# Kernel optimization log

Hardware: AMD Instinct MI355X
Metric: run time of the kernel (lower is better)

The kernel has to match this reference:

```python
import jax, jax.numpy as jnp
import numpy as np

N_NODES = 50000
N_EDGES = 800000
D_IN = 128
D_OUT = 128


def setup_inputs() -> dict:
    key = jax.random.key(0)
    k1, k2, k3 = jax.random.split(key, 3)
    x = jax.random.normal(k1, (N_NODES, D_IN), dtype=jnp.float32)
    edge_index = jax.random.randint(k2, (2, N_EDGES), 0, N_NODES, dtype=jnp.int64)
    # glorot init for weight, zeros for bias
    limit = float(np.sqrt(6.0 / (D_IN + D_OUT)))
    W = jax.random.uniform(k3, (D_IN, D_OUT), dtype=jnp.float32, minval=-limit, maxval=limit)
    b = jnp.zeros((D_OUT,), dtype=jnp.float32)
    return {"x": x, "edge_index": edge_index, "W": W, "b": b}


def reference(x, edge_index, W, b):
    # GCNConv forward: dense transform, then sym-normalized propagation with self-loops.
    N = x.shape[0]
    h = x @ W  # [N, D_OUT]

    src = edge_index[0]
    dst = edge_index[1]
    # add self loops (fill weight = 1.0 since improved=False)
    loop = jnp.arange(N, dtype=src.dtype)
    src = jnp.concatenate([src, loop])
    dst = jnp.concatenate([dst, loop])
    ew = jnp.ones(src.shape[0], dtype=h.dtype)

    # sym normalization: D^{-1/2} A D^{-1/2}
    deg = jax.ops.segment_sum(ew, dst, num_segments=N)  # [N]
    deg_inv_sqrt = jnp.where(deg > 0, jax.lax.rsqrt(jnp.maximum(deg, 1e-12)), 0.0)
    norm = deg_inv_sqrt[src] * ew * deg_inv_sqrt[dst]  # [E+N]

    # message = norm * x_j ; aggregate = scatter-add to dst
    msg = norm[:, None] * h[src]  # [E+N, D_OUT]
    out = jax.ops.segment_sum(msg, dst, num_segments=N)  # [N, D_OUT]
    return out + b
```

## Files before the change

### kernel.cpp

```cpp
#include <hip/hip_runtime.h>
#include <math.h>

#define N_NODES 50000
#define N_EDGES 800000
#define D 128
#define NBKT 392
#define CHUNK 4096
#define NCHUNK ((N_EDGES + CHUNK - 1) / CHUNK)
#define CAPB 4096
#define GEMM_BLOCKS ((N_NODES + 63) / 64)

typedef short bf16x8 __attribute__((ext_vector_type(8)));
typedef float f32x4 __attribute__((ext_vector_type(4)));

static __device__ __forceinline__ unsigned short f2bf_rn(float f) {
    unsigned u = __float_as_uint(f);
    unsigned r = (u + 0x7FFF + ((u >> 16) & 1)) >> 16;
    return (unsigned short)r;
}
static __device__ __forceinline__ float bf2f(unsigned short h) {
    return __uint_as_float(((unsigned)h) << 16);
}


__global__ __launch_bounds__(256) void setup(const float* __restrict__ W,
                                             unsigned short* __restrict__ wH,
                                             int* __restrict__ gcur,
                                             int* __restrict__ row_start) {
    if (blockIdx.x < 8) {
        int tid = blockIdx.x * 256 + threadIdx.x;
        int kstep = tid >> 9;
        int ct = (tid >> 6) & 7;
        int lane = tid & 63;
        int kbase = kstep * 32 + ((lane >> 4) << 3);
        int c = ct * 16 + (lane & 15);
        #pragma unroll
        for (int e = 0; e < 8; ++e) {
            wH[tid * 8 + e] = f2bf_rn(W[(kbase + e) * 128 + c]);
        }
    } else {
        for (int j = threadIdx.x; j < NBKT; j += 256) gcur[j] = j * CAPB;
        if (threadIdx.x == 0) row_start[N_NODES] = N_EDGES;
    }
}


__global__ __launch_bounds__(256) void part_gemm(const int* __restrict__ ei,
                                                 int* __restrict__ gcur,
                                                 unsigned int* __restrict__ part,
                                                 const float* __restrict__ x,
                                                 const unsigned short* __restrict__ wH,
                                                 unsigned short* __restrict__ h) {
    __shared__ unsigned int ebuf[CHUNK];
    __shared__ unsigned int obuf[CHUNK];
    __shared__ int hist[NBKT];
    __shared__ int spos[NBKT];
    __shared__ int goff[NBKT];
    __shared__ int sm[256];
    int t = threadIdx.x;

    if (blockIdx.x < NCHUNK) {
        int base = blockIdx.x * CHUNK;
        int n = N_EDGES - base; if (n > CHUNK) n = CHUNK;

        for (int j = t; j < NBKT; j += 256) hist[j] = 0;
        __syncthreads();
        for (int i = t; i < n; i += 256) {
            unsigned s = (unsigned)ei[base + i];
            unsigned d = (unsigned)ei[N_EDGES + base + i];
            ebuf[i] = s | (d << 16);
            atomicAdd(&hist[d >> 7], 1);
        }
        __syncthreads();
        int i0 = 2 * t, i1 = i0 + 1;
        int a = (i0 < NBKT) ? hist[i0] : 0;
        int b = (i1 < NBKT) ? hist[i1] : 0;
        int ps = a + b;
        sm[t] = ps; __syncthreads();
        for (int o = 1; o < 256; o <<= 1) {
            int ad = (t >= o) ? sm[t - o] : 0;
            __syncthreads();
            sm[t] += ad;
            __syncthreads();
        }
        int ex = sm[t] - ps;
        if (i0 < NBKT) spos[i0] = ex;
        if (i1 < NBKT) spos[i1] = ex + a;
        __syncthreads();
        for (int j = t; j < NBKT; j += 256) {
            int gp = atomicAdd(&gcur[j], hist[j]);
            goff[j] = gp - spos[j];
        }
        __syncthreads();
        for (int j = t; j < NBKT; j += 256) hist[j] = 0;
        __syncthreads();
        for (int i = t; i < n; i += 256) {
            unsigned e = ebuf[i];
            int bk = e >> 23;
            int p = spos[bk] + atomicAdd(&hist[bk], 1);
            obuf[p] = e;
        }
        __syncthreads();
        for (int i = t; i < n; i += 256) {
            unsigned e = obuf[i];
            int bk = e >> 23;
            part[goff[bk] + i] = e;
        }
    } else {
        int gb = blockIdx.x - NCHUNK;
        int wave = t >> 6;
        int lane = t & 63;
        int rowbase = gb * 64 + wave * 16;

        f32x4 acc[8];
        #pragma unroll
        for (int ct = 0; ct < 8; ++ct) acc[ct] = (f32x4)(0.f);

        int arow = rowbase + (lane & 15);
        if (arow >= N_NODES) arow = N_NODES - 1;
        const float* xrow = x + (size_t)arow * 128 + ((lane >> 4) << 3);

        #pragma unroll
        for (int kstep = 0; kstep < 4; ++kstep) {
            float4 a0 = *(const float4*)(xrow + kstep * 32);
            float4 a1 = *(const float4*)(xrow + kstep * 32 + 4);
            float av[8] = {a0.x, a0.y, a0.z, a0.w, a1.x, a1.y, a1.z, a1.w};
            bf16x8 ah, al;
            #pragma unroll
            for (int e = 0; e < 8; ++e) {
                unsigned short hb = f2bf_rn(av[e]);
                float res = av[e] - bf2f(hb);
                ah[e] = (short)hb;
                al[e] = (short)f2bf_rn(res);
            }
            const bf16x8* bh = (const bf16x8*)(wH + (size_t)(kstep * 8) * 64 * 8 + lane * 8);
            #pragma unroll
            for (int ct = 0; ct < 8; ++ct) {
                bf16x8 bhv = bh[ct * 64];
                acc[ct] = __builtin_amdgcn_mfma_f32_16x16x32_bf16(ah, bhv, acc[ct], 0, 0, 0);
                acc[ct] = __builtin_amdgcn_mfma_f32_16x16x32_bf16(al, bhv, acc[ct], 0, 0, 0);
            }
        }

        int rbase = rowbase + ((lane >> 4) << 2);
        int col = lane & 15;
        #pragma unroll
        for (int ct = 0; ct < 8; ++ct) {
            #pragma unroll
            for (int i = 0; i < 4; ++i) {
                int row = rbase + i;
                if (row < N_NODES) h[(size_t)row * 128 + ct * 16 + col] = f2bf_rn(acc[ct][i]);
            }
        }
    }
}


__global__ __launch_bounds__(256) void csr_build(const unsigned int* __restrict__ part,
                                                 const int* __restrict__ gcur,
                                                 int* __restrict__ row_start,
                                                 float* __restrict__ dinv,
                                                 unsigned short* __restrict__ ssrc16) {
    __shared__ unsigned int ebuf[CAPB];
    __shared__ unsigned short img[CAPB];
    __shared__ int exf[NBKT];
    __shared__ int sm2[256];
    __shared__ int h128[128];
    __shared__ int loff[128];
    __shared__ int sm[128];
    int t = threadIdx.x;
    int b = blockIdx.x;

    int i0 = 2 * t, i1 = i0 + 1;
    int a = (i0 < NBKT) ? (gcur[i0] - i0 * CAPB) : 0;
    int b2 = (i1 < NBKT) ? (gcur[i1] - i1 * CAPB) : 0;
    int ps = a + b2;
    sm2[t] = ps; __syncthreads();
    for (int o = 1; o < 256; o <<= 1) {
        int ad = (t >= o) ? sm2[t - o] : 0;
        __syncthreads();
        sm2[t] += ad;
        __syncthreads();
    }
    int ex = sm2[t] - ps;
    if (i0 < NBKT) exf[i0] = ex;
    if (i1 < NBKT) exf[i1] = ex + a;
    for (int j = t; j < 128; j += 256) h128[j] = 0;
    __syncthreads();

    int cnt = gcur[b] - b * CAPB;
    int cb = exf[b];
    int gb = b * CAPB;
    int nbase = b * 128;

    for (int i = t; i < cnt; i += 256) {
        unsigned e = part[gb + i];
        ebuf[i] = e;
        atomicAdd(&h128[(e >> 16) & 127], 1);
    }
    __syncthreads();
    if (t < 128) sm[t] = h128[t];
    __syncthreads();
    for (int o = 1; o < 128; o <<= 1) {
        int ad = 0;
        if (t < 128 && t >= o) ad = sm[t - o];
        __syncthreads();
        if (t < 128) sm[t] += ad;
        __syncthreads();
    }
    if (t < 128) {
        int exl = sm[t] - h128[t];
        loff[t] = exl;
        int node = nbase + t;
        if (node < N_NODES) {
            row_start[node] = cb + exl;
            dinv[node] = rsqrtf((float)(h128[t] + 1));
        }
        h128[t] = 0;
    }
    __syncthreads();
    for (int i = t; i < cnt; i += 256) {
        unsigned e = ebuf[i];
        int j = (e >> 16) & 127;
        int p = loff[j] + atomicAdd(&h128[j], 1);
        img[p] = (unsigned short)(e & 0xffffu);
    }
    __syncthreads();
    for (int i = t; i < cnt; i += 256) ssrc16[cb + i] = img[i];
}


__global__ __launch_bounds__(256) void aggregate(const unsigned int* __restrict__ hu,
                                                 const int* __restrict__ row_start,
                                                 const unsigned short* __restrict__ ssrc16,
                                                 const float* __restrict__ dinv,
                                                 const float* __restrict__ bias,
                                                 float* __restrict__ out) {
    int node = blockIdx.x * 4 + (threadIdx.x >> 6);
    int lane = threadIdx.x & 63;
    if (node >= N_NODES) return;
    int s = row_start[node];
    int t = row_start[node + 1];
    float accx = 0.f, accy = 0.f;
    for (int base = s; base < t; base += 64) {
        int c = t - base;
        if (c > 64) c = 64;
        int li = base + (lane < c ? lane : c - 1);
        int idx = (int)ssrc16[li];
        float dv = dinv[idx];
        int j = 0;
        for (; j + 8 <= c; j += 8) {
            int ss[8]; float dd[8]; unsigned uu[8];
            #pragma unroll
            for (int k = 0; k < 8; ++k) {
                ss[k] = __shfl(idx, j + k);
                dd[k] = __shfl(dv, j + k);
            }
            #pragma unroll
            for (int k = 0; k < 8; ++k) uu[k] = hu[(size_t)ss[k] * 64 + lane];
            #pragma unroll
            for (int k = 0; k < 8; ++k) {
                accx += dd[k] * __uint_as_float(uu[k] << 16);
                accy += dd[k] * __uint_as_float(uu[k] & 0xffff0000u);
            }
        }
        for (; j < c; ++j) {
            int sj = __shfl(idx, j);
            float dj = __shfl(dv, j);
            unsigned u = hu[(size_t)sj * 64 + lane];
            accx += dj * __uint_as_float(u << 16);
            accy += dj * __uint_as_float(u & 0xffff0000u);
        }
    }
    float di = dinv[node];
    unsigned us = hu[(size_t)node * 64 + lane];
    float2 bv = *(const float2*)&bias[2 * lane];
    float2 o;
    o.x = di * accx + di * di * __uint_as_float(us << 16) + bv.x;
    o.y = di * accy + di * di * __uint_as_float(us & 0xffff0000u) + bv.y;
    *(float2*)&out[(size_t)node * 128 + 2 * lane] = o;
}


extern "C" void kernel_launch(void* const* d_in, const int* in_sizes, int n_in,
                              void* d_out, int out_size, void* d_ws, size_t ws_size,
                              hipStream_t stream) {
    const float* x  = (const float*)d_in[0];
    const int*   ei = (const int*)d_in[1];
    const float* W  = (const float*)d_in[2];
    const float* b  = (const float*)d_in[3];
    float* out = (float*)d_out;

    char* ws = (char*)d_ws;
    unsigned short* h      = (unsigned short*)(ws + 0);
    int*   row_start       = (int*)  (ws + 12800000);
    float* dinv            = (float*)(ws + 13000016);
    unsigned short* ssrc16 = (unsigned short*)(ws + 13200016);
    int*   gcur            = (int*)  (ws + 14800016);
    unsigned short* wH     = (unsigned short*)(ws + 14801600);
    unsigned int*   part   = (unsigned int*)  (ws + 14834368);

    hipLaunchKernelGGL(setup,     dim3(9),                    dim3(256), 0, stream, W, wH, gcur, row_start);
    hipLaunchKernelGGL(part_gemm, dim3(NCHUNK + GEMM_BLOCKS), dim3(256), 0, stream,
                       ei, gcur, part, x, wH, h);
    hipLaunchKernelGGL(csr_build, dim3(NBKT),                 dim3(256), 0, stream, part, gcur, row_start, dinv, ssrc16);
    hipLaunchKernelGGL(aggregate, dim3((N_NODES + 3) / 4),    dim3(256), 0, stream,
                       (const unsigned int*)h, row_start, ssrc16, dinv, b, out);
}
```

Before: 137.8 us.

## Simplify edge bucketing to register-held entries with atomic-returned ranks

The partition phase now keeps each thread's 16 packed edges in registers and uses the value returned by the shared histogram atomicAdd as the edge's rank within its bucket. This removes the LDS staging buffers, the block-wide prefix scan, the second histogram pass and the local reorder. Global writes into the partition array become scattered within buckets rather than contiguous runs from the sorted local buffer. It also frees about 33KB of LDS, which may raise occupancy of the fused part/GEMM kernel.

```diff
diff --git a/kernel.cpp b/kernel.cpp
--- a/kernel.cpp
+++ b/kernel.cpp
@@ -51,12 +51,8 @@
                                                  const float* __restrict__ x,
                                                  const unsigned short* __restrict__ wH,
                                                  unsigned short* __restrict__ h) {
-    __shared__ unsigned int ebuf[CHUNK];
-    __shared__ unsigned int obuf[CHUNK];
     __shared__ int hist[NBKT];
-    __shared__ int spos[NBKT];
     __shared__ int goff[NBKT];
-    __shared__ int sm[256];
     int t = threadIdx.x;
 
     if (blockIdx.x < NCHUNK) {
@@ -65,46 +61,32 @@
 
         for (int j = t; j < NBKT; j += 256) hist[j] = 0;
         __syncthreads();
-        for (int i = t; i < n; i += 256) {
-            unsigned s = (unsigned)ei[base + i];
-            unsigned d = (unsigned)ei[N_EDGES + base + i];
-            ebuf[i] = s | (d << 16);
-            atomicAdd(&hist[d >> 7], 1);
-        }
-        __syncthreads();
-        int i0 = 2 * t, i1 = i0 + 1;
-        int a = (i0 < NBKT) ? hist[i0] : 0;
-        int b = (i1 < NBKT) ? hist[i1] : 0;
-        int ps = a + b;
-        sm[t] = ps; __syncthreads();
-        for (int o = 1; o < 256; o <<= 1) {
-            int ad = (t >= o) ? sm[t - o] : 0;
-            __syncthreads();
-            sm[t] += ad;
-            __syncthreads();
-        }
-        int ex = sm[t] - ps;
-        if (i0 < NBKT) spos[i0] = ex;
-        if (i1 < NBKT) spos[i1] = ex + a;
+
+        unsigned eregs[16];
+        int rregs[16];
+        #pragma unroll
+        for (int k = 0; k < 16; ++k) {
+            int i = t + k * 256;
+            if (i < n) {
+                unsigned s = (unsigned)ei[base + i];
+                unsigned d = (unsigned)ei[N_EDGES + base + i];
+                unsigned e = s | (d << 16);
+                eregs[k] = e;
+                rregs[k] = atomicAdd(&hist[d >> 7], 1);
+            }
+        }
         __syncthreads();
         for (int j = t; j < NBKT; j += 256) {
-            int gp = atomicAdd(&gcur[j], hist[j]);
-            goff[j] = gp - spos[j];
-        }
-        __syncthreads();
-        for (int j = t; j < NBKT; j += 256) hist[j] = 0;
-        __syncthreads();
-        for (int i = t; i < n; i += 256) {
-            unsigned e = ebuf[i];
-            int bk = e >> 23;
-            int p = spos[bk] + atomicAdd(&hist[bk], 1);
-            obuf[p] = e;
-        }
-        __syncthreads();
-        for (int i = t; i < n; i += 256) {
-            unsigned e = obuf[i];
-            int bk = e >> 23;
-            part[goff[bk] + i] = e;
+            goff[j] = atomicAdd(&gcur[j], hist[j]);
+        }
+        __syncthreads();
+        #pragma unroll
+        for (int k = 0; k < 16; ++k) {
+            int i = t + k * 256;
+            if (i < n) {
+                unsigned e = eregs[k];
+                part[goff[e >> 23] + rregs[k]] = e;
+            }
         }
     } else {
         int gb = blockIdx.x - NCHUNK;
```

After: 139.4 us. About the same (+1.2%).
